# Performance work log

Measured on AMD Instinct MI355X. Metric: run time of the kernel, lower is better.

The kernel has to match this reference:

```python
import jax, jax.numpy as jnp
import numpy as np

B, IN, HID, LAT, EH = 32768, 512, 2048, 128, 512
MID = max(HID // 2, LAT * 2)      # 1024
HALF = max(EH // 2, 4)            # 256
EPS = 1e-5
LN10 = float(np.log(10.0))


def setup_inputs() -> dict:
    key = jax.random.key(0)
    ks = jax.random.split(key, 24)
    r = lambda k, shp, s=0.02: (jax.random.normal(k, shp, dtype=jnp.float32) * s)
    d = {
        "x": jax.random.normal(ks[0], (B, IN), dtype=jnp.float32),
        "group_idx": jax.random.randint(ks[1], (B,), 0, 3),
        # encoder: Linear(IN,HID)+BN+ELU, Linear(HID,MID)+BN+ELU, Linear(MID,LAT)
        "e_w1": r(ks[2], (HID, IN)), "e_b1": jnp.zeros((HID,), jnp.float32),
        "e_g1": jnp.ones((HID,), jnp.float32), "e_be1": jnp.zeros((HID,), jnp.float32),
        "e_w2": r(ks[3], (MID, HID)), "e_b2": jnp.zeros((MID,), jnp.float32),
        "e_g2": jnp.ones((MID,), jnp.float32), "e_be2": jnp.zeros((MID,), jnp.float32),
        "e_w3": r(ks[4], (LAT, MID)), "e_b3": jnp.zeros((LAT,), jnp.float32),
        # shared: Linear(LAT+IN,HID)+BN+ELU, Linear(HID,MID)+BN+ELU
        "s_w1": r(ks[5], (HID, LAT + IN)), "s_b1": jnp.zeros((HID,), jnp.float32),
        "s_g1": jnp.ones((HID,), jnp.float32), "s_be1": jnp.zeros((HID,), jnp.float32),
        "s_w2": r(ks[6], (MID, HID)), "s_b2": jnp.zeros((MID,), jnp.float32),
        "s_g2": jnp.ones((MID,), jnp.float32), "s_be2": jnp.zeros((MID,), jnp.float32),
        # 3 expert heads, stacked on leading axis E=3
        "h_w1": r(ks[7], (3, EH, MID)), "h_b1": jnp.zeros((3, EH), jnp.float32),
        "h_w2": r(ks[8], (3, HALF, EH)), "h_b2": jnp.zeros((3, HALF), jnp.float32),
        "h_w3": r(ks[9], (3, HALF)), "h_b3": jnp.zeros((3,), jnp.float32),
    }
    return d


def _bn(h, g, b):
    # BatchNorm1d in training mode: batch mean, biased batch var
    m = jnp.mean(h, axis=0)
    v = jnp.var(h, axis=0)
    return (h - m) * (g / jnp.sqrt(v + EPS)) + b


def _elu(h):
    return jax.nn.elu(h)


def reference(x, group_idx,
              e_w1, e_b1, e_g1, e_be1, e_w2, e_b2, e_g2, e_be2, e_w3, e_b3,
              s_w1, s_b1, s_g1, s_be1, s_w2, s_b2, s_g2, s_be2,
              h_w1, h_b1, h_w2, h_b2, h_w3, h_b3):
    # encoder
    h = _elu(_bn(x @ e_w1.T + e_b1, e_g1, e_be1))
    h = _elu(_bn(h @ e_w2.T + e_b2, e_g2, e_be2))
    latent = h @ e_w3.T + e_b3                              # [B, LAT]
    # shared trunk
    z = jnp.concatenate([latent, x], axis=-1)               # [B, LAT+IN]
    h = _elu(_bn(z @ s_w1.T + s_b1, s_g1, s_be1))
    hidden = _elu(_bn(h @ s_w2.T + s_b2, s_g2, s_be2))      # [B, MID]
    # expert heads: compute all 3 (tiny vs trunk), then select per-row group
    t1 = _elu(jnp.einsum('bm,ehm->ebh', hidden, h_w1) + h_b1[:, None, :])   # [3,B,EH]
    t2 = _elu(jnp.einsum('ebh,efh->ebf', t1, h_w2) + h_b2[:, None, :])      # [3,B,HALF]
    pred_all = jnp.einsum('ebf,ef->eb', t2, h_w3) + h_b3[:, None]           # [3,B]
    pred_raw = jnp.take_along_axis(pred_all, group_idx[None, :], axis=0)[0] # [B]
    pred_log = -jax.nn.softplus(pred_raw)
    pred_prob = jnp.exp(pred_log * jnp.float32(LN10))       # 10 ** pred_log
    return pred_log, pred_prob
```

## Files before the change

kernel.cpp:

```cpp
#include <hip/hip_runtime.h>
#include <math.h>

#define B_    32768
#define LN10_ 2.302585092994046f
#define MT_H  264
#define NBLK  128

typedef __attribute__((ext_vector_type(8))) short short8;
typedef __attribute__((ext_vector_type(4))) float f32x4;

typedef const __attribute__((address_space(1))) void gvoid_t;
typedef __attribute__((address_space(3))) void svoid_t;

__device__ __forceinline__ void gl16(const void* g, void* l) {
  __builtin_amdgcn_global_load_lds((gvoid_t*)g, (svoid_t*)l, 16, 0, 0);
}

__device__ __forceinline__ float bf2f(unsigned int u) {
  union { unsigned int i; float f; } v; v.i = u << 16; return v.f;
}
__device__ __forceinline__ unsigned short f2bf(float f) {
  union { float f; unsigned int i; } v; v.f = f;
  unsigned int x = v.i;
  unsigned int r = x + 0x7FFFu + ((x >> 16) & 1u);
  return (unsigned short)(r >> 16);
}

__global__ __launch_bounds__(256)
void gemm_bt(const unsigned short* __restrict__ A0, int lda,
             const unsigned short* __restrict__ W0, int ldw,
             unsigned short* __restrict__ C0, int ldc,
             int K, const float* __restrict__ bias0, int elu,
             float* __restrict__ st, int Ntot,
             long eA, long eW, long eC, int eBias,
             const int* __restrict__ texp) {
  __shared__ __align__(16) unsigned short lA[128 * 64];
  __shared__ __align__(16) unsigned short lB[128 * 64];
  const int t = threadIdx.x;
  const int nx = gridDim.x, ny = gridDim.y;
  const int f = blockIdx.y * nx + blockIdx.x;
  const int xcd = f & 7, g = f >> 3;
  const int gdiv = g / nx;
  const int mt = xcd * (ny >> 3) + gdiv;
  const int nt = g - gdiv * nx;
  const int mBase = mt * 128;
  const int nBase = nt * 128;
  int e = texp ? texp[mt] : (int)blockIdx.z;
  if (e < 0) return;
  const unsigned short* A = A0 + (size_t)e * eA;
  const unsigned short* W = W0 + (size_t)e * eW;
  unsigned short* C = C0 + (size_t)e * eC;
  const float* bias = bias0 ? (bias0 + (size_t)e * eBias) : nullptr;
  const unsigned short* Ap = A + (size_t)mBase * lda;
  const unsigned short* Wp = W + (size_t)nBase * ldw;
  const int w = t >> 6, l = t & 63;
  const int wr = (w >> 1) * 64, wc = (w & 1) * 64;
  const int lm = l & 15, lg = l >> 4;

  f32x4 acc[4][4];
#pragma unroll
  for (int i = 0; i < 4; ++i)
#pragma unroll
    for (int j = 0; j < 4; ++j) {
      f32x4 z4 = {0.f, 0.f, 0.f, 0.f};
      acc[i][j] = z4;
    }

  for (int k0 = 0; k0 < K; k0 += 64) {
    __syncthreads();
#pragma unroll
    for (int it = 0; it < 4; ++it) {
      int chunk = it * 256 + t;
      int row = chunk >> 3, sc = chunk & 7;
      int gc = (sc ^ (row & 7)) << 3;
      gl16(Ap + (size_t)row * lda + k0 + gc, &lA[chunk * 8]);
      gl16(Wp + (size_t)row * ldw + k0 + gc, &lB[chunk * 8]);
    }
    __syncthreads();
#pragma unroll
    for (int kk = 0; kk < 64; kk += 32) {
      short8 af[4], bfr[4];
#pragma unroll
      for (int i = 0; i < 4; ++i) {
        int ar = wr + i * 16 + lm;
        int ac = (kk >> 3) + lg;
        af[i] = *(const short8*)&lA[ar * 64 + ((ac ^ (ar & 7)) << 3)];
      }
#pragma unroll
      for (int j = 0; j < 4; ++j) {
        int br = wc + j * 16 + lm;
        int bc = (kk >> 3) + lg;
        bfr[j] = *(const short8*)&lB[br * 64 + ((bc ^ (br & 7)) << 3)];
      }
#pragma unroll
      for (int i = 0; i < 4; ++i)
#pragma unroll
        for (int j = 0; j < 4; ++j)
          acc[i][j] = __builtin_amdgcn_mfma_f32_16x16x32_bf16(af[i], bfr[j], acc[i][j], 0, 0, 0);
    }
  }

#pragma unroll
  for (int j = 0; j < 4; ++j) {
    int n = nBase + wc + j * 16 + lm;
    float bj = bias ? bias[n] : 0.f;
    float s = 0.f, q = 0.f;
#pragma unroll
    for (int i = 0; i < 4; ++i) {
      int m0 = mBase + wr + i * 16 + lg * 4;
#pragma unroll
      for (int r = 0; r < 4; ++r) {
        float v = acc[i][j][r] + bj;
        if (elu) v = v > 0.f ? v : expm1f(v);
        s += v; q += v * v;
        C[(size_t)(m0 + r) * ldc + n] = f2bf(v);
      }
    }
    if (st) {
      s += __shfl_xor(s, 16, 64); s += __shfl_xor(s, 32, 64);
      q += __shfl_xor(q, 16, 64); q += __shfl_xor(q, 32, 64);
      if (lg == 0) { atomicAdd(&st[n], s); atomicAdd(&st[Ntot + n], q); }
    }
  }
}

__global__ void bn_apply(unsigned short* __restrict__ Y, const float* __restrict__ st,
                         const float* __restrict__ gam, const float* __restrict__ bet,
                         int N, float invB) {
  size_t i = (size_t)blockIdx.x * blockDim.x + threadIdx.x;
  size_t base = i * 8;
  int col = (int)(base & (size_t)(N - 1));
  float a8[8], b8[8];
#pragma unroll
  for (int k = 0; k < 8; ++k) {
    int c = col + k;
    float m = st[c] * invB;
    float var = st[N + c] * invB - m * m;
    float av = gam[c] * rsqrtf(var + 1e-5f);
    a8[k] = av;
    b8[k] = bet[c] - m * av;
  }
  uint4 u = *(uint4*)&Y[base];
  unsigned int uu[4] = {u.x, u.y, u.z, u.w};
  unsigned int oo[4];
#pragma unroll
  for (int k = 0; k < 4; ++k) {
    float vlo = bf2f(uu[k] & 0xFFFFu);
    float vhi = bf2f(uu[k] >> 16);
    float flo = a8[2 * k] * vlo + b8[2 * k];
    float fhi = a8[2 * k + 1] * vhi + b8[2 * k + 1];
    flo = flo > 0.f ? flo : expm1f(flo);
    fhi = fhi > 0.f ? fhi : expm1f(fhi);
    oo[k] = (unsigned int)f2bf(flo) | ((unsigned int)f2bf(fhi) << 16);
  }
  uint4 o = {oo[0], oo[1], oo[2], oo[3]};
  *(uint4*)&Y[base] = o;
}

__global__ void cast_all(const float* __restrict__ e1, const float* __restrict__ e2,
                         const float* __restrict__ e3, const float* __restrict__ s1,
                         const float* __restrict__ s2, const float* __restrict__ h1,
                         const float* __restrict__ h2, unsigned short* __restrict__ dst) {
  int i4 = blockIdx.x * 256 + threadIdx.x;
  const float* src;
  int rel;
  if (i4 < 786432) {
    if (i4 < 262144) { src = e1; rel = i4; }
    else             { src = e2; rel = i4 - 262144; }
  } else if (i4 < 1146880) {
    if (i4 < 819200) { src = e3; rel = i4 - 786432; }
    else             { src = s1; rel = i4 - 819200; }
  } else if (i4 < 2064384) {
    if (i4 < 1671168) { src = s2; rel = i4 - 1146880; }
    else              { src = h1; rel = i4 - 1671168; }
  } else { src = h2; rel = i4 - 2064384; }
  float4 v = ((const float4*)src)[rel];
  ushort4 o = {f2bf(v.x), f2bf(v.y), f2bf(v.z), f2bf(v.w)};
  ((ushort4*)dst)[i4] = o;
}

__global__ void cast_x(const float* __restrict__ x, unsigned short* __restrict__ z) {
  int i = blockIdx.x * blockDim.x + threadIdx.x;
  int b = i >> 7;
  int c = (i & 127) << 2;
  float4 v = *(const float4*)&x[(size_t)b * 512 + c];
  ushort4 o = {f2bf(v.x), f2bf(v.y), f2bf(v.z), f2bf(v.w)};
  *(ushort4*)&z[(size_t)b * 640 + 128 + c] = o;
}

__global__ void hist_blocks(const int* __restrict__ gidx, int* __restrict__ bcnt) {
  int blk = blockIdx.x;
  int i = blk * 256 + threadIdx.x;
  int e = gidx[i];
  int l = threadIdx.x & 63, w = threadIdx.x >> 6;
  __shared__ int wc[4][3];
  unsigned long long m0 = __ballot(e == 0);
  unsigned long long m1 = __ballot(e == 1);
  unsigned long long m2 = __ballot(e == 2);
  if (l == 0) { wc[w][0] = __popcll(m0); wc[w][1] = __popcll(m1); wc[w][2] = __popcll(m2); }
  __syncthreads();
  if (threadIdx.x < 3)
    bcnt[blk * 3 + threadIdx.x] = wc[0][threadIdx.x] + wc[1][threadIdx.x] +
                                  wc[2][threadIdx.x] + wc[3][threadIdx.x];
}

__global__ void scan_plan(const int* __restrict__ bcnt, int* __restrict__ boff,
                          int* __restrict__ vend, int* __restrict__ texp) {
  __shared__ int sp[4];
  __shared__ int cnt[3];
  int t = threadIdx.x;
  if (t < 3) {
    int s = 0;
    for (int b = 0; b < NBLK; ++b) s += bcnt[b * 3 + t];
    cnt[t] = s;
  }
  __syncthreads();
  if (t == 0) {
    int p = 0;
    for (int e = 0; e < 3; ++e) {
      sp[e] = p; vend[e] = p + cnt[e];
      p += ((cnt[e] + 127) >> 7) << 7;
    }
    sp[3] = p;
  }
  __syncthreads();
  if (t < 3) {
    int run = sp[t];
    for (int b = 0; b < NBLK; ++b) { boff[b * 3 + t] = run; run += bcnt[b * 3 + t]; }
  }
  if (t < MT_H) {
    int r0 = t << 7, e = -1;
    for (int k = 0; k < 3; ++k)
      if (r0 >= sp[k] && r0 < sp[k + 1]) e = k;
    texp[t] = e;
  }
}

__global__ void scatter2(const int* __restrict__ gidx, const int* __restrict__ boff,
                         int* __restrict__ perm) {
  int blk = blockIdx.x;
  int i = blk * 256 + threadIdx.x;
  int e = gidx[i];
  int l = threadIdx.x & 63, w = threadIdx.x >> 6;
  __shared__ int wc[4][3];
  unsigned long long m0 = __ballot(e == 0);
  unsigned long long m1 = __ballot(e == 1);
  unsigned long long m2 = __ballot(e == 2);
  if (l == 0) { wc[w][0] = __popcll(m0); wc[w][1] = __popcll(m1); wc[w][2] = __popcll(m2); }
  __syncthreads();
  unsigned long long me = (e == 0) ? m0 : ((e == 1) ? m1 : m2);
  int rank = __popcll(me & ((1ull << l) - 1ull));
  int woff = 0;
  for (int ww = 0; ww < w; ++ww) woff += wc[ww][e];
  perm[boff[blk * 3 + e] + woff + rank] = i;
}

__global__ void gather_h(const unsigned short* __restrict__ hid, const int* __restrict__ perm,
                         const int* __restrict__ texp, const int* __restrict__ vend,
                         unsigned short* __restrict__ ht) {
  int idx = blockIdx.x * 256 + threadIdx.x;
  int p = idx >> 7, c8 = (idx & 127) << 3;
  int e = texp[p >> 7];
  uint4 v = {0u, 0u, 0u, 0u};
  if (e >= 0 && p < vend[e]) {
    int src = perm[p];
    v = *(const uint4*)&hid[(size_t)src * 1024 + c8];
  }
  *(uint4*)&ht[(size_t)p * 1024 + c8] = v;
}

__global__ void final_pred(const unsigned short* __restrict__ t2, const int* __restrict__ perm,
                           const int* __restrict__ texp, const int* __restrict__ vend,
                           const float* __restrict__ w3, const float* __restrict__ b3,
                           float* __restrict__ out) {
  int p = blockIdx.x * 4 + (threadIdx.x >> 6);
  int l = threadIdx.x & 63;
  int e = texp[p >> 7];
  if (e < 0 || p >= vend[e]) return;
  ushort4 u = *(const ushort4*)&t2[(size_t)p * 256 + l * 4];
  float4 wv = *(const float4*)&w3[e * 256 + l * 4];
  float sum = bf2f(u.x) * wv.x + bf2f(u.y) * wv.y + bf2f(u.z) * wv.z + bf2f(u.w) * wv.w;
#pragma unroll
  for (int off = 32; off; off >>= 1) sum += __shfl_down(sum, off, 64);
  if (l == 0) {
    int orig = perm[p];
    float xr = sum + b3[e];
    float sp = (xr > 0.f) ? (xr + log1pf(expf(-xr))) : log1pf(expf(xr));
    float pl = -sp;
    out[orig] = pl;
    out[B_ + orig] = expf(pl * LN10_);
  }
}

extern "C" void kernel_launch(void* const* d_in, const int* in_sizes, int n_in,
                              void* d_out, int out_size, void* d_ws, size_t ws_size,
                              hipStream_t stream) {
  const float* x    = (const float*)d_in[0];
  const int*   gidx = (const int*)d_in[1];
  const float* e_w1 = (const float*)d_in[2];
  const float* e_g1 = (const float*)d_in[4];
  const float* e_be1= (const float*)d_in[5];
  const float* e_w2 = (const float*)d_in[6];
  const float* e_g2 = (const float*)d_in[8];
  const float* e_be2= (const float*)d_in[9];
  const float* e_w3 = (const float*)d_in[10];
  const float* e_b3 = (const float*)d_in[11];
  const float* s_w1 = (const float*)d_in[12];
  const float* s_g1 = (const float*)d_in[14];
  const float* s_be1= (const float*)d_in[15];
  const float* s_w2 = (const float*)d_in[16];
  const float* s_g2 = (const float*)d_in[18];
  const float* s_be2= (const float*)d_in[19];
  const float* h_w1 = (const float*)d_in[20];
  const float* h_b1 = (const float*)d_in[21];
  const float* h_w2 = (const float*)d_in[22];
  const float* h_b2 = (const float*)d_in[23];
  const float* h_w3 = (const float*)d_in[24];
  const float* h_b3 = (const float*)d_in[25];
  float* out = (float*)d_out;

  char* ws = (char*)d_ws;
  size_t off = 0;
  auto alloc = [&](size_t bytes) -> char* {
    char* p = ws + off;
    off += (bytes + 255) & ~(size_t)255;
    return p;
  };
  unsigned short* wb_e1 = (unsigned short*)alloc((size_t)2048 * 512 * 2);
  unsigned short* wb_e2 = (unsigned short*)alloc((size_t)1024 * 2048 * 2);
  unsigned short* wb_e3 = (unsigned short*)alloc((size_t)128 * 1024 * 2);
  unsigned short* wb_s1 = (unsigned short*)alloc((size_t)2048 * 640 * 2);
  unsigned short* wb_s2 = (unsigned short*)alloc((size_t)1024 * 2048 * 2);
  unsigned short* wb_h1 = (unsigned short*)alloc((size_t)3 * 512 * 1024 * 2);
  unsigned short* wb_h2 = (unsigned short*)alloc((size_t)3 * 256 * 512 * 2);
  unsigned short* z     = (unsigned short*)alloc((size_t)B_ * 640 * 2);
  unsigned short* bufA  = (unsigned short*)alloc((size_t)B_ * 2048 * 2);
  unsigned short* bufB  = (unsigned short*)alloc((size_t)B_ * 1024 * 2);
  float* st = (float*)alloc(12288 * sizeof(float));
  float* st0 = st;
  float* st1 = st + 4096;
  float* st2 = st + 6144;
  float* st3 = st + 10240;
  int* bcnt = (int*)alloc(NBLK * 3 * sizeof(int));
  int* boff = (int*)alloc(NBLK * 3 * sizeof(int));
  int* vend = (int*)alloc(3 * sizeof(int));
  int* texp = (int*)alloc(MT_H * sizeof(int));
  int* perm = (int*)alloc((size_t)MT_H * 128 * sizeof(int));
  unsigned short* ht  = bufA;
  unsigned short* t1p = bufA + (size_t)MT_H * 128 * 1024;
  unsigned short* t2p = z;

  cast_all<<<8448, 256, 0, stream>>>(e_w1, e_w2, e_w3, s_w1, s_w2, h_w1, h_w2, wb_e1);
  cast_x<<<(B_ * 128) / 256, 256, 0, stream>>>(x, z);
  hipMemsetAsync(st, 0, 12288 * sizeof(float), stream);
  hist_blocks<<<NBLK, 256, 0, stream>>>(gidx, bcnt);
  scan_plan<<<1, 512, 0, stream>>>(bcnt, boff, vend, texp);
  scatter2<<<NBLK, 256, 0, stream>>>(gidx, boff, perm);

  gemm_bt<<<dim3(16, 256), 256, 0, stream>>>(z + 128, 640, wb_e1, 512, bufA, 2048, 512,
                                             nullptr, 0, st0, 2048, 0, 0, 0, 0, nullptr);
  bn_apply<<<B_, 256, 0, stream>>>(bufA, st0, e_g1, e_be1, 2048, 1.0f / B_);
  gemm_bt<<<dim3(8, 256), 256, 0, stream>>>(bufA, 2048, wb_e2, 2048, bufB, 1024, 2048,
                                            nullptr, 0, st1, 1024, 0, 0, 0, 0, nullptr);
  bn_apply<<<B_ / 2, 256, 0, stream>>>(bufB, st1, e_g2, e_be2, 1024, 1.0f / B_);
  gemm_bt<<<dim3(1, 256), 256, 0, stream>>>(bufB, 1024, wb_e3, 1024, z, 640, 1024,
                                            e_b3, 0, nullptr, 0, 0, 0, 0, 0, nullptr);
  gemm_bt<<<dim3(16, 256), 256, 0, stream>>>(z, 640, wb_s1, 640, bufA, 2048, 640,
                                             nullptr, 0, st2, 2048, 0, 0, 0, 0, nullptr);
  bn_apply<<<B_, 256, 0, stream>>>(bufA, st2, s_g1, s_be1, 2048, 1.0f / B_);
  gemm_bt<<<dim3(8, 256), 256, 0, stream>>>(bufA, 2048, wb_s2, 2048, bufB, 1024, 2048,
                                            nullptr, 0, st3, 1024, 0, 0, 0, 0, nullptr);
  bn_apply<<<B_ / 2, 256, 0, stream>>>(bufB, st3, s_g2, s_be2, 1024, 1.0f / B_);

  gather_h<<<(MT_H * 128 * 128) / 256, 256, 0, stream>>>(bufB, perm, texp, vend, ht);

  gemm_bt<<<dim3(4, MT_H), 256, 0, stream>>>(ht, 1024, wb_h1, 1024, t1p, 512, 1024,
                                             h_b1, 1, nullptr, 0,
                                             0, (long)512 * 1024, 0, 512, texp);
  gemm_bt<<<dim3(2, MT_H), 256, 0, stream>>>(t1p, 512, wb_h2, 512, t2p, 256, 512,
                                             h_b2, 1, nullptr, 0,
                                             0, (long)256 * 512, 0, 256, texp);

  final_pred<<<(MT_H * 128) / 4, 256, 0, stream>>>(t2p, perm, texp, vend, h_w3, h_b3, out);
}
```

Baseline: 1.158 ms.

## Add 256x256-tile, 4-stage pipelined GEMM for the four large trunk layers

Adds a new GEMM kernel with 512 threads and a 256x256 output tile. It uses a 4-deep LDS ring filled by global_load_lds, explicit vmcnt waits, and setprio around the MFMA block. The kernel replaces the 128x128 gemm_bt for the four big encoder and shared-trunk GEMMs. The aim is higher arithmetic intensity per LDS byte and better overlap of loads with MFMA work, at the cost of 128 KB of LDS, heavy register use for 32 accumulators, and half as many blocks.

```diff
diff --git a/kernel.cpp b/kernel.cpp
--- a/kernel.cpp
+++ b/kernel.cpp
@@ -25,6 +25,106 @@
   unsigned int r = x + 0x7FFFu + ((x >> 16) & 1u);
   return (unsigned short)(r >> 16);
 }
+
+#define SLB 16384
+
+__global__ __launch_bounds__(512)
+void gemm256(const unsigned short* __restrict__ A0, int lda,
+             const unsigned short* __restrict__ W0, int ldw,
+             unsigned short* __restrict__ C0, int ldc, int K,
+             float* __restrict__ st, int Ntot) {
+  __shared__ __align__(16) unsigned short lds[4 * SLB];
+  const int t = threadIdx.x;
+  const int nx = gridDim.x, ny = gridDim.y;
+  const int f = blockIdx.y * nx + blockIdx.x;
+  const int xcd = f & 7, g = f >> 3;
+  const int gdiv = g / nx;
+  const int mt = xcd * (ny >> 3) + gdiv;
+  const int nt = g - gdiv * nx;
+  const int mBase = mt * 256, nBase = nt * 256;
+  const unsigned short* Ap = A0 + (size_t)mBase * lda;
+  const unsigned short* Wp = W0 + (size_t)nBase * ldw;
+  const int w = t >> 6, l = t & 63;
+  const int wr = w >> 2, wc = w & 3;
+  const int lm = l & 15, lg = l >> 4;
+
+  const int srow = ((t >> 6) << 4) + (t & 15);
+  const int skch = (t >> 4) & 3;
+  const unsigned short* gA0 = Ap + (size_t)srow * lda + skch * 8;
+  const unsigned short* gA1 = Ap + (size_t)(srow + 128) * lda + skch * 8;
+  const unsigned short* gB0 = Wp + (size_t)srow * ldw + skch * 8;
+  const unsigned short* gB1 = Wp + (size_t)(srow + 128) * ldw + skch * 8;
+
+#define STAGE(ss)                                                         \
+  {                                                                       \
+    const int bo_ = ((ss) & 3) * SLB;                                     \
+    const size_t ko_ = (size_t)(ss) * 32;                                 \
+    gl16(gA0 + ko_, &lds[bo_ + t * 8]);                                   \
+    gl16(gA1 + ko_, &lds[bo_ + 4096 + t * 8]);                            \
+    gl16(gB0 + ko_, &lds[bo_ + 8192 + t * 8]);                            \
+    gl16(gB1 + ko_, &lds[bo_ + 12288 + t * 8]);                           \
+  }
+
+  f32x4 acc[8][4];
+#pragma unroll
+  for (int i = 0; i < 8; ++i)
+#pragma unroll
+    for (int j = 0; j < 4; ++j) {
+      f32x4 z4 = {0.f, 0.f, 0.f, 0.f};
+      acc[i][j] = z4;
+    }
+
+  const int NS = K >> 5;
+  STAGE(0); STAGE(1); STAGE(2);
+
+#define GBODY(ss, dostage)                                                \
+  {                                                                       \
+    __builtin_amdgcn_s_barrier();                                         \
+    __builtin_amdgcn_sched_barrier(0);                                    \
+    const int bo = ((ss) & 3) * SLB;                                      \
+    short8 af[8], bq[4];                                                  \
+    _Pragma("unroll") for (int i = 0; i < 8; ++i)                         \
+        af[i] = *(const short8*)&lds[bo + wr * 4096 + i * 512 + l * 8];   \
+    _Pragma("unroll") for (int j = 0; j < 4; ++j)                         \
+        bq[j] = *(const short8*)&lds[bo + 8192 + wc * 2048 + j * 512 + l * 8]; \
+    if (dostage) STAGE((ss) + 3);                                         \
+    __builtin_amdgcn_s_setprio(1);                                        \
+    _Pragma("unroll") for (int i = 0; i < 8; ++i)                         \
+      _Pragma("unroll") for (int j = 0; j < 4; ++j)                       \
+        acc[i][j] = __builtin_amdgcn_mfma_f32_16x16x32_bf16(af[i], bq[j], acc[i][j], 0, 0, 0); \
+    __builtin_amdgcn_s_setprio(0);                                        \
+  }
+
+  for (int s = 0; s + 2 < NS; ++s) {
+    asm volatile("s_waitcnt vmcnt(8)" ::: "memory");
+    GBODY(s, s + 3 < NS);
+  }
+  asm volatile("s_waitcnt vmcnt(4)" ::: "memory");
+  GBODY(NS - 2, false);
+  asm volatile("s_waitcnt vmcnt(0)" ::: "memory");
+  GBODY(NS - 1, false);
+
+#pragma unroll
+  for (int j = 0; j < 4; ++j) {
+    int n = nBase + wc * 64 + j * 16 + lm;
+    float s1 = 0.f, q1 = 0.f;
+#pragma unroll
+    for (int i = 0; i < 8; ++i) {
+      int m0 = mBase + wr * 128 + i * 16 + lg * 4;
+#pragma unroll
+      for (int r = 0; r < 4; ++r) {
+        float v = acc[i][j][r];
+        s1 += v; q1 += v * v;
+        C0[(size_t)(m0 + r) * ldc + n] = f2bf(v);
+      }
+    }
+    s1 += __shfl_xor(s1, 16, 64); s1 += __shfl_xor(s1, 32, 64);
+    q1 += __shfl_xor(q1, 16, 64); q1 += __shfl_xor(q1, 32, 64);
+    if (lg == 0) { atomicAdd(&st[n], s1); atomicAdd(&st[Ntot + n], q1); }
+  }
+}
+#undef STAGE
+#undef GBODY
 
 __global__ __launch_bounds__(256)
 void gemm_bt(const unsigned short* __restrict__ A0, int lda,
@@ -357,19 +457,19 @@
   scan_plan<<<1, 512, 0, stream>>>(bcnt, boff, vend, texp);
   scatter2<<<NBLK, 256, 0, stream>>>(gidx, boff, perm);
 
-  gemm_bt<<<dim3(16, 256), 256, 0, stream>>>(z + 128, 640, wb_e1, 512, bufA, 2048, 512,
-                                             nullptr, 0, st0, 2048, 0, 0, 0, 0, nullptr);
+  gemm256<<<dim3(8, 128), 512, 0, stream>>>(z + 128, 640, wb_e1, 512, bufA, 2048, 512,
+                                            st0, 2048);
   bn_apply<<<B_, 256, 0, stream>>>(bufA, st0, e_g1, e_be1, 2048, 1.0f / B_);
-  gemm_bt<<<dim3(8, 256), 256, 0, stream>>>(bufA, 2048, wb_e2, 2048, bufB, 1024, 2048,
-                                            nullptr, 0, st1, 1024, 0, 0, 0, 0, nullptr);
+  gemm256<<<dim3(4, 128), 512, 0, stream>>>(bufA, 2048, wb_e2, 2048, bufB, 1024, 2048,
+                                            st1, 1024);
   bn_apply<<<B_ / 2, 256, 0, stream>>>(bufB, st1, e_g2, e_be2, 1024, 1.0f / B_);
   gemm_bt<<<dim3(1, 256), 256, 0, stream>>>(bufB, 1024, wb_e3, 1024, z, 640, 1024,
                                             e_b3, 0, nullptr, 0, 0, 0, 0, 0, nullptr);
-  gemm_bt<<<dim3(16, 256), 256, 0, stream>>>(z, 640, wb_s1, 640, bufA, 2048, 640,
-                                             nullptr, 0, st2, 2048, 0, 0, 0, 0, nullptr);
+  gemm256<<<dim3(8, 128), 512, 0, stream>>>(z, 640, wb_s1, 640, bufA, 2048, 640,
+                                            st2, 2048);
   bn_apply<<<B_, 256, 0, stream>>>(bufA, st2, s_g1, s_be1, 2048, 1.0f / B_);
-  gemm_bt<<<dim3(8, 256), 256, 0, stream>>>(bufA, 2048, wb_s2, 2048, bufB, 1024, 2048,
-                                            nullptr, 0, st3, 1024, 0, 0, 0, 0, nullptr);
+  gemm256<<<dim3(4, 128), 512, 0, stream>>>(bufA, 2048, wb_s2, 2048, bufB, 1024, 2048,
+                                            st3, 1024);
   bn_apply<<<B_ / 2, 256, 0, stream>>>(bufB, st3, s_g2, s_be2, 1024, 1.0f / B_);
 
   gather_h<<<(MT_H * 128 * 128) / 256, 256, 0, stream>>>(bufB, perm, texp, vend, ht);
```

Result: faster. 1.102 ms (-4.9%).
